# Performance work log

Measured on AMD Instinct MI355X. Metric: run time of the kernel, lower is better.

Reference implementation:

```python
import jax, jax.numpy as jnp
import numpy as np

N_CELLS, N_CLASSES, N_GENES, N_EDGES, HID = 100000, 50, 500, 600000, 8
NEG_SLOPE = 0.2  # GATv2Conv default negative_slope


def setup_inputs() -> dict:
    key = jax.random.key(0)
    ks = jax.random.split(key, 10)
    X = jax.random.normal(ks[0], (N_CELLS, N_GENES), jnp.float32)
    Mu = jax.random.normal(ks[1], (N_CLASSES, N_GENES), jnp.float32)
    # variances must be strictly positive
    Var = jax.random.uniform(ks[2], (N_CLASSES, N_GENES), jnp.float32) + 0.5
    W = 0.1 * jax.random.normal(ks[3], (N_CELLS, N_CLASSES), jnp.float32)
    S = 1.0 + 0.05 * jax.random.normal(ks[4], (N_CELLS, 1), jnp.float32)
    edge_index = jax.random.randint(ks[5], (2, N_EDGES), 0, N_CELLS, jnp.int32)
    sc = 1.0 / np.sqrt(N_GENES)
    lin_l_w = sc * jax.random.normal(ks[6], (HID, N_GENES), jnp.float32)
    lin_l_b = jnp.zeros((HID,), jnp.float32)
    lin_r_w = sc * jax.random.normal(ks[7], (HID, N_GENES), jnp.float32)
    lin_r_b = jnp.zeros((HID,), jnp.float32)
    att = jax.random.normal(ks[8], (HID,), jnp.float32) / np.sqrt(HID)
    return dict(X=X, Mu=Mu, Var=Var, W=W, S=S, edge_index=edge_index,
                lin_l_w=lin_l_w, lin_l_b=lin_l_b,
                lin_r_w=lin_r_w, lin_r_b=lin_r_b, att=att)


def _forward(X, Mu, Var, W, S, lin_l_w, lin_l_b, lin_r_w, lin_r_b, att, edge_index):
    N = X.shape[0]
    P = jax.nn.softmax(W, axis=1)  # [N, C]

    # Gaussian log-likelihood term.
    # F[n,c] = -0.5 * sum_g (X[n,g] - Mu[c,g]*S[n])^2 / Var[c,g]
    # Expanded into GEMMs (algebraically identical, avoids the [N,C,G] intermediate):
    invV = 1.0 / Var                          # [C, G]
    t1 = (X * X) @ invV.T                     # [N, C]  sum_g X^2/Var
    t2 = X @ (Mu * invV).T                    # [N, C]  sum_g X*Mu/Var
    t3 = jnp.sum(Mu * Mu * invV, axis=1)      # [C]     sum_g Mu^2/Var
    Fmat = -0.5 * (t1 - 2.0 * S * t2 + (S * S) * t3[None, :])  # [N, C]
    ll_prot = jnp.sum(P * Fmat) / N

    # GATv2 attention coefficients (heads=1, add_self_loops=False).
    gl = X @ lin_l_w.T + lin_l_b              # [N, HID]  lin_l (source side)
    gr = X @ lin_r_w.T + lin_r_b              # [N, HID]  lin_r (target side)
    src, dst = edge_index[0], edge_index[1]
    e = jax.nn.leaky_relu(gl[src] + gr[dst], NEG_SLOPE)  # [E, HID]
    score = e @ att                                       # [E]
    # segment softmax over destination nodes
    m = jax.ops.segment_max(score, dst, num_segments=N)
    ex = jnp.exp(score - m[dst])
    denom = jax.ops.segment_sum(ex, dst, num_segments=N)
    alpha = ex / denom[dst]                               # [E]

    ce_space = -jnp.sum(P[src] * alpha[:, None] * jnp.log(P[dst] + 1e-8)) / N
    return ll_prot, ce_space, P


def reference(X, Mu, Var, W, S, edge_index, lin_l_w, lin_l_b, lin_r_w, lin_r_b, att):
    return _forward(X, Mu, Var, W, S, lin_l_w, lin_l_b, lin_r_w, lin_r_b, att, edge_index)
```

## Files before the change

### kernel.cpp

```cpp
#include <hip/hip_runtime.h>
#include <math.h>

#define N_CELLS   100000
#define N_CLASSES 50
#define N_GENES   500
#define N_EDGES   600000
#define HID       8
#define NKT       8
#define NB_FUSED  1563
#define NB_CE     391
#define PROWS     56

typedef __attribute__((ext_vector_type(4))) float f32x4;
typedef __attribute__((ext_vector_type(8))) short bf16x8;
typedef __attribute__((ext_vector_type(8))) unsigned short u16x8;

static const size_t OFF_BF    = 0;
static const size_t OFF_T3    = 147456;
static const size_t OFF_GLR   = 147712;
static const size_t OFF_PB    = 6547712;
static const size_t OFF_LQ    = 17747712;
static const size_t OFF_DENOM = 28947712;
static const size_t OFF_NUMER = 29347712;
static const size_t OFF_LLP   = 29747712;
static const size_t OFF_CEP   = 29754112;
static const size_t ZERO_BEG  = OFF_DENOM;
static const size_t ZERO_BYTES= 29747712 - 28947712;

__device__ __forceinline__ ushort f2bf(float f) {
    union { float f; unsigned u; } v; v.f = f;
    unsigned r = v.u + 0x7fffu + ((v.u >> 16) & 1u);
    return (ushort)(r >> 16);
}
__device__ __forceinline__ float bf2f(ushort b) {
    union { unsigned u; float f; } v; v.u = ((unsigned)b) << 16; return v.f;
}
__device__ __forceinline__ unsigned cvt_pk_bf16(float lo, float hi) {
    unsigned r;
    asm("v_cvt_pk_bf16_f32 %0, %1, %2" : "=v"(r) : "v"(lo), "v"(hi));
    return r;
}
__device__ __forceinline__ void gload16(const void* g, void* l) {
    __builtin_amdgcn_global_load_lds(
        (const __attribute__((address_space(1))) unsigned int*)g,
        (__attribute__((address_space(3))) unsigned int*)l,
        16, 0, 0);
}

__global__ __launch_bounds__(256) void k_prep(const float* __restrict__ Var,
                                              const float* __restrict__ Mu,
                                              const float* __restrict__ wl,
                                              const float* __restrict__ wr,
                                              ushort* __restrict__ Bf,
                                              float* __restrict__ t3) {
    if (blockIdx.x < 288) {
        int id = blockIdx.x * 256 + threadIdx.x;
        float v = 0.f;
        if (id < 65536) {
            int e    = id & 7;
            int lane = (id >> 3) & 63;
            int j    = (id >> 9) & 15;
            int kt   = id >> 13;
            int t    = j >> 1, ss = j & 1;
            int s    = kt * 2 + ss;
            int k    = s * 32 + ((lane >> 4) << 3) + e;
            int c    = (t & 3) * 16 + (lane & 15);
            if (k < N_GENES && c < N_CLASSES)
                v = (t < 4) ? 1.0f / Var[c * N_GENES + k]
                            : Mu[c * N_GENES + k] / Var[c * N_GENES + k];
        } else {
            int rem  = id - 65536;
            int e    = rem & 7;
            int lane = (rem >> 3) & 63;
            int s    = rem >> 9;
            int k    = s * 32 + ((lane >> 4) << 3) + e;
            int h    = lane & 15;
            if (k < N_GENES)
                v = (h < HID) ? wl[h * N_GENES + k] : wr[(h - HID) * N_GENES + k];
        }
        Bf[id] = f2bf(v);
    } else {
        int c    = (blockIdx.x - 288) * 4 + (threadIdx.x >> 6);
        int lane = threadIdx.x & 63;
        if (c >= N_CLASSES) return;
        float s = 0.f;
        for (int g = lane; g < N_GENES; g += 64) {
            float m = Mu[c * N_GENES + g];
            s += m * m / Var[c * N_GENES + g];
        }
        #pragma unroll
        for (int off = 32; off; off >>= 1) s += __shfl_xor(s, off);
        if (lane == 0) t3[c] = s;
    }
}

__global__ __launch_bounds__(256) void k_softmax(const float* __restrict__ W,
                                                 float* __restrict__ P,
                                                 ushort* __restrict__ Pb,
                                                 ushort* __restrict__ LQ) {
    int wid  = (blockIdx.x * 256 + threadIdx.x) >> 6;
    int lane = threadIdx.x & 63;
    if (wid >= N_CELLS) return;
    float w = (lane < N_CLASSES) ? W[(size_t)wid * N_CLASSES + lane] : -__builtin_inff();
    float m = w;
    #pragma unroll
    for (int off = 32; off; off >>= 1) m = fmaxf(m, __shfl_xor(m, off));
    float e = (lane < N_CLASSES) ? expf(w - m) : 0.f;
    float s = e;
    #pragma unroll
    for (int off = 32; off; off >>= 1) s += __shfl_xor(s, off);
    float p = e / s;
    if (lane < N_CLASSES) P[(size_t)wid * N_CLASSES + lane] = p;
    if (lane < PROWS) {
        Pb[(size_t)wid * PROWS + lane] = (lane < N_CLASSES) ? f2bf(p) : 0;
        LQ[(size_t)wid * PROWS + lane] = (lane < N_CLASSES) ? f2bf(logf(p + 1e-8f)) : 0;
    }
}

__global__ __launch_bounds__(256, 2) void k_fused(const float* __restrict__ X,
                                                  const float* __restrict__ S,
                                                  const float* __restrict__ P,
                                                  const ushort* __restrict__ Bf,
                                                  const float* __restrict__ t3,
                                                  const float* __restrict__ bl,
                                                  const float* __restrict__ br,
                                                  ushort* __restrict__ glrb,
                                                  float* __restrict__ llp) {
    __shared__ float  ldsA[2][4][16][16][4];
    __shared__ ushort ldsB[2][20][64][8];
    __shared__ float  wsum[4];
    int tid  = threadIdx.x;
    int lane = tid & 63;
    int wv   = tid >> 6;
    int lhi  = lane >> 4;
    int slot = lane & 15;
    int rbase = blockIdx.x * 64 + wv * 16;
    const char* Xc  = (const char*)X;
    const char* Bfc = (const char*)Bf;

    int arow = rbase + slot;
    if (arow > N_CELLS - 1) arow = N_CELLS - 1;
    float m2s = -2.0f * S[arow];

    const f32x4 zz = {0.f, 0.f, 0.f, 0.f};
    f32x4 acc1[4], acc2[4], acc3;
    #pragma unroll
    for (int ct = 0; ct < 4; ++ct) { acc1[ct] = zz; acc2[ct] = zz; }
    acc3 = zz;

#define STAGE(KT, BUF) do {                                                        \
    _Pragma("unroll")                                                              \
    for (int i = 0; i < 4; ++i) {                                                  \
        int rloc = i * 4 + lhi;                                                    \
        int row  = rbase + rloc; if (row > N_CELLS - 1) row = N_CELLS - 1;         \
        int gi   = (KT) * 16 + (slot ^ (rloc & 7)); if (gi > 124) gi = 124;        \
        gload16(Xc + (size_t)row * 2000 + (size_t)gi * 16, &ldsA[BUF][wv][i * 4][0][0]); \
    }                                                                              \
    _Pragma("unroll")                                                              \
    for (int i = 0; i < 5; ++i) {                                                  \
        int j = wv * 5 + i;                                                        \
        size_t src;                                                                \
        if (j < 16)      src = (size_t)(KT) * 16384 + (size_t)j * 1024;            \
        else if (j < 18) src = 131072 + ((size_t)(KT) * 2 + (size_t)(j - 16)) * 1024; \
        else             src = (size_t)(KT) * 16384;                               \
        gload16(Bfc + src + (size_t)lane * 16, &ldsB[BUF][j][0][0]);               \
    }                                                                              \
} while (0)

    STAGE(0, 0);

    #pragma unroll
    for (int kt = 0; kt < NKT; ++kt) {
        const int cur = kt & 1;
        if (kt < NKT - 1) {
            STAGE(kt + 1, cur ^ 1);
            __builtin_amdgcn_sched_barrier(0);
            asm volatile("s_waitcnt vmcnt(9)" ::: "memory");
        } else {
            __builtin_amdgcn_sched_barrier(0);
            asm volatile("s_waitcnt vmcnt(0)" ::: "memory");
        }
        __builtin_amdgcn_sched_barrier(0);
        __builtin_amdgcn_s_barrier();
        __builtin_amdgcn_sched_barrier(0);

        const bf16x8* BL = (const bf16x8*)&ldsB[cur][0][0][0];
        #pragma unroll
        for (int ks = 0; ks < 2; ++ks) {
            int key = slot & 7;
            int c0  = ks * 8 + lhi * 2;
            f32x4 xa = *(const f32x4*)&ldsA[cur][wv][slot][c0 ^ key][0];
            f32x4 xb = *(const f32x4*)&ldsA[cur][wv][slot][(c0 + 1) ^ key][0];
            union { bf16x8 v; unsigned u[4]; } a1, a2;
            a1.u[0] = cvt_pk_bf16(xa[0] * xa[0], xa[1] * xa[1]);
            a1.u[1] = cvt_pk_bf16(xa[2] * xa[2], xa[3] * xa[3]);
            a1.u[2] = cvt_pk_bf16(xb[0] * xb[0], xb[1] * xb[1]);
            a1.u[3] = cvt_pk_bf16(xb[2] * xb[2], xb[3] * xb[3]);
            a2.u[0] = cvt_pk_bf16(m2s * xa[0], m2s * xa[1]);
            a2.u[1] = cvt_pk_bf16(m2s * xa[2], m2s * xa[3]);
            a2.u[2] = cvt_pk_bf16(m2s * xb[0], m2s * xb[1]);
            a2.u[3] = cvt_pk_bf16(m2s * xb[2], m2s * xb[3]);
            bf16x8 bg = BL[(16 + ks) * 64 + lane];
            #pragma unroll
            for (int ct = 0; ct < 4; ++ct)
                acc1[ct] = __builtin_amdgcn_mfma_f32_16x16x32_bf16(a1.v, BL[(ct * 2 + ks) * 64 + lane], acc1[ct], 0, 0, 0);
            #pragma unroll
            for (int ct = 0; ct < 4; ++ct)
                acc2[ct] = __builtin_amdgcn_mfma_f32_16x16x32_bf16(a2.v, BL[((4 + ct) * 2 + ks) * 64 + lane], acc2[ct], 0, 0, 0);
            acc3 = __builtin_amdgcn_mfma_f32_16x16x32_bf16(a2.v, bg, acc3, 0, 0, 0);
        }
        __builtin_amdgcn_sched_barrier(0);
        __builtin_amdgcn_s_barrier();
        __builtin_amdgcn_sched_barrier(0);
    }
#undef STAGE

    int col = lane & 15;
    int rg  = lane >> 4;
    float bias = (col < HID) ? bl[col] : br[col - HID];
    float part = 0.f;
    #pragma unroll
    for (int r = 0; r < 4; ++r) {
        int row = rbase + rg * 4 + r;
        if (row < N_CELLS) {
            float s2 = S[row];
            glrb[(size_t)row * 16 + col] = f2bf(acc3[r] / (-2.0f * s2) + bias);
            float ss = s2 * s2;
            #pragma unroll
            for (int ct = 0; ct < 4; ++ct) {
                int c = ct * 16 + col;
                if (c < N_CLASSES) {
                    float F = -0.5f * (acc1[ct][r] + acc2[ct][r] + ss * t3[c]);
                    part = fmaf(P[(size_t)row * N_CLASSES + c], F, part);
                }
            }
        }
    }
    #pragma unroll
    for (int off = 32; off; off >>= 1) part += __shfl_xor(part, off);
    if (lane == 0) wsum[wv] = part;
    __syncthreads();
    if (tid == 0) llp[blockIdx.x] = wsum[0] + wsum[1] + wsum[2] + wsum[3];
}

__global__ __launch_bounds__(256) void k_edge(const int* __restrict__ ei,
                                              const ushort* __restrict__ glrb,
                                              const float* __restrict__ att,
                                              const ushort* __restrict__ Pb,
                                              const ushort* __restrict__ LQ,
                                              float* __restrict__ denom,
                                              float* __restrict__ numer) {
    int e = blockIdx.x * 256 + threadIdx.x;
    if (e >= N_EDGES) return;
    int src = ei[e], dst = ei[N_EDGES + e];
    u16x8 gv = *(const u16x8*)(glrb + (size_t)src * 16);
    u16x8 hv = *(const u16x8*)(glrb + (size_t)dst * 16 + 8);
    const float4* at = (const float4*)att;
    float4 a0 = at[0], a1 = at[1];
    float t, s = 0.f;
    t = bf2f(gv[0]) + bf2f(hv[0]); t = t > 0.f ? t : 0.2f * t; s = fmaf(a0.x, t, s);
    t = bf2f(gv[1]) + bf2f(hv[1]); t = t > 0.f ? t : 0.2f * t; s = fmaf(a0.y, t, s);
    t = bf2f(gv[2]) + bf2f(hv[2]); t = t > 0.f ? t : 0.2f * t; s = fmaf(a0.z, t, s);
    t = bf2f(gv[3]) + bf2f(hv[3]); t = t > 0.f ? t : 0.2f * t; s = fmaf(a0.w, t, s);
    t = bf2f(gv[4]) + bf2f(hv[4]); t = t > 0.f ? t : 0.2f * t; s = fmaf(a1.x, t, s);
    t = bf2f(gv[5]) + bf2f(hv[5]); t = t > 0.f ? t : 0.2f * t; s = fmaf(a1.y, t, s);
    t = bf2f(gv[6]) + bf2f(hv[6]); t = t > 0.f ? t : 0.2f * t; s = fmaf(a1.z, t, s);
    t = bf2f(gv[7]) + bf2f(hv[7]); t = t > 0.f ? t : 0.2f * t; s = fmaf(a1.w, t, s);
    float ex = expf(s);

    const u16x8* ps = (const u16x8*)(Pb + (size_t)src * PROWS);
    const u16x8* ld = (const u16x8*)(LQ + (size_t)dst * PROWS);
    float v = 0.f;
    #pragma unroll
    for (int i = 0; i < 7; ++i) {
        u16x8 pv = ps[i], lv = ld[i];
        #pragma unroll
        for (int j = 0; j < 8; ++j)
            v = fmaf(bf2f(pv[j]), bf2f(lv[j]), v);
    }
    atomicAdd(denom + dst, ex);
    atomicAdd(numer + dst, ex * v);
}

__global__ __launch_bounds__(256) void k_ce(const float* __restrict__ denom,
                                            const float* __restrict__ numer,
                                            float* __restrict__ cep) {
    __shared__ float wsum[4];
    int n = blockIdx.x * 256 + threadIdx.x;
    float v = 0.f;
    if (n < N_CELLS) {
        float d = denom[n];
        v = (d > 0.f) ? numer[n] / d : 0.f;
    }
    #pragma unroll
    for (int off = 32; off; off >>= 1) v += __shfl_xor(v, off);
    if ((threadIdx.x & 63) == 0) wsum[threadIdx.x >> 6] = v;
    __syncthreads();
    if (threadIdx.x == 0) cep[blockIdx.x] = wsum[0] + wsum[1] + wsum[2] + wsum[3];
}

__global__ __launch_bounds__(256) void k_reduce(const float* __restrict__ llp,
                                                const float* __restrict__ cep,
                                                float* __restrict__ out) {
    __shared__ double l1[256], l2[256];
    int t = threadIdx.x;
    double s1 = 0.0, s2 = 0.0;
    for (int i = t; i < NB_FUSED; i += 256) s1 += (double)llp[i];
    for (int i = t; i < NB_CE; i += 256) s2 += (double)cep[i];
    l1[t] = s1; l2[t] = s2;
    __syncthreads();
    for (int off = 128; off; off >>= 1) {
        if (t < off) { l1[t] += l1[t + off]; l2[t] += l2[t + off]; }
        __syncthreads();
    }
    if (t == 0) {
        out[0] = (float)(l1[0] / (double)N_CELLS);
        out[1] = (float)(-l2[0] / (double)N_CELLS);
    }
}

extern "C" void kernel_launch(void* const* d_in, const int* in_sizes, int n_in,
                              void* d_out, int out_size, void* d_ws, size_t ws_size,
                              hipStream_t stream) {
    const float* X   = (const float*)d_in[0];
    const float* Mu  = (const float*)d_in[1];
    const float* Var = (const float*)d_in[2];
    const float* W   = (const float*)d_in[3];
    const float* S   = (const float*)d_in[4];
    const int*   ei  = (const int*)d_in[5];
    const float* wl  = (const float*)d_in[6];
    const float* bl  = (const float*)d_in[7];
    const float* wr  = (const float*)d_in[8];
    const float* br  = (const float*)d_in[9];
    const float* att = (const float*)d_in[10];
    float* out = (float*)d_out;
    char*  ws  = (char*)d_ws;

    ushort* Bf    = (ushort*)(ws + OFF_BF);
    float*  t3    = (float*)(ws + OFF_T3);
    ushort* glrb  = (ushort*)(ws + OFF_GLR);
    ushort* Pb    = (ushort*)(ws + OFF_PB);
    ushort* LQ    = (ushort*)(ws + OFF_LQ);
    float*  denom = (float*)(ws + OFF_DENOM);
    float*  numer = (float*)(ws + OFF_NUMER);
    float*  llp   = (float*)(ws + OFF_LLP);
    float*  cep   = (float*)(ws + OFF_CEP);
    float*  P     = out + 2;

    hipMemsetAsync(ws + ZERO_BEG, 0, ZERO_BYTES, stream);

    k_prep   <<<301, 256, 0, stream>>>(Var, Mu, wl, wr, Bf, t3);
    k_softmax<<<(N_CELLS * 64 + 255) / 256, 256, 0, stream>>>(W, P, Pb, LQ);
    k_fused  <<<NB_FUSED, 256, 0, stream>>>(X, S, P, Bf, t3, bl, br, glrb, llp);
    k_edge   <<<(N_EDGES + 255) / 256, 256, 0, stream>>>(ei, glrb, att, Pb, LQ, denom, numer);
    k_ce     <<<NB_CE, 256, 0, stream>>>(denom, numer, cep);
    k_reduce <<<1, 256, 0, stream>>>(llp, cep, out);
}
```

Before: 179.1 us.

## Merge prep, softmax and memset into one kernel; fold final reduce via ticket

Replaces the memset, prep and softmax launches with a single k_front kernel. Its first blocks zero the denom/numer accumulators and the ticket, build the bf16 B tiles and t3, and the remaining blocks compute the row softmax. The separate final reduction kernel is removed: the last k_ce block, found with an atomic ticket counter, does the double-precision reduction. This cuts three launches and their inter-kernel gaps, at the cost of threadfence/atomic overhead and a serial tail in the last block.

```diff
diff --git a/kernel.cpp b/kernel.cpp
--- a/kernel.cpp
+++ b/kernel.cpp
@@ -24,8 +24,7 @@
 static const size_t OFF_NUMER = 29347712;
 static const size_t OFF_LLP   = 29747712;
 static const size_t OFF_CEP   = 29754112;
-static const size_t ZERO_BEG  = OFF_DENOM;
-static const size_t ZERO_BYTES= 29747712 - 28947712;
+static const size_t OFF_TKT   = 29755904;
 
 __device__ __forceinline__ ushort f2bf(float f) {
     union { float f; unsigned u; } v; v.f = f;
@@ -47,12 +46,23 @@
         16, 0, 0);
 }
 
-__global__ __launch_bounds__(256) void k_prep(const float* __restrict__ Var,
-                                              const float* __restrict__ Mu,
-                                              const float* __restrict__ wl,
-                                              const float* __restrict__ wr,
-                                              ushort* __restrict__ Bf,
-                                              float* __restrict__ t3) {
+__global__ __launch_bounds__(256) void k_front(const float* __restrict__ Var,
+                                               const float* __restrict__ Mu,
+                                               const float* __restrict__ wl,
+                                               const float* __restrict__ wr,
+                                               const float* __restrict__ W,
+                                               ushort* __restrict__ Bf,
+                                               float* __restrict__ t3,
+                                               float* __restrict__ P,
+                                               ushort* __restrict__ Pb,
+                                               ushort* __restrict__ LQ,
+                                               unsigned* __restrict__ zeroed,
+                                               unsigned* __restrict__ ticket) {
+    if (blockIdx.x < 301) {
+        int gid = blockIdx.x * 256 + threadIdx.x;
+        for (int i = gid; i < 200000; i += 77056) zeroed[i] = 0u;
+        if (gid == 0) *ticket = 0u;
+    }
     if (blockIdx.x < 288) {
         int id = blockIdx.x * 256 + threadIdx.x;
         float v = 0.f;
@@ -79,7 +89,7 @@
                 v = (h < HID) ? wl[h * N_GENES + k] : wr[(h - HID) * N_GENES + k];
         }
         Bf[id] = f2bf(v);
-    } else {
+    } else if (blockIdx.x < 301) {
         int c    = (blockIdx.x - 288) * 4 + (threadIdx.x >> 6);
         int lane = threadIdx.x & 63;
         if (c >= N_CLASSES) return;
@@ -91,29 +101,23 @@
         #pragma unroll
         for (int off = 32; off; off >>= 1) s += __shfl_xor(s, off);
         if (lane == 0) t3[c] = s;
-    }
-}
-
-__global__ __launch_bounds__(256) void k_softmax(const float* __restrict__ W,
-                                                 float* __restrict__ P,
-                                                 ushort* __restrict__ Pb,
-                                                 ushort* __restrict__ LQ) {
-    int wid  = (blockIdx.x * 256 + threadIdx.x) >> 6;
-    int lane = threadIdx.x & 63;
-    if (wid >= N_CELLS) return;
-    float w = (lane < N_CLASSES) ? W[(size_t)wid * N_CLASSES + lane] : -__builtin_inff();
-    float m = w;
-    #pragma unroll
-    for (int off = 32; off; off >>= 1) m = fmaxf(m, __shfl_xor(m, off));
-    float e = (lane < N_CLASSES) ? expf(w - m) : 0.f;
-    float s = e;
-    #pragma unroll
-    for (int off = 32; off; off >>= 1) s += __shfl_xor(s, off);
-    float p = e / s;
-    if (lane < N_CLASSES) P[(size_t)wid * N_CLASSES + lane] = p;
-    if (lane < PROWS) {
-        Pb[(size_t)wid * PROWS + lane] = (lane < N_CLASSES) ? f2bf(p) : 0;
-        LQ[(size_t)wid * PROWS + lane] = (lane < N_CLASSES) ? f2bf(logf(p + 1e-8f)) : 0;
+    } else {
+        int wid  = (blockIdx.x - 301) * 4 + (threadIdx.x >> 6);
+        int lane = threadIdx.x & 63;
+        float w = (lane < N_CLASSES) ? W[(size_t)wid * N_CLASSES + lane] : -__builtin_inff();
+        float m = w;
+        #pragma unroll
+        for (int off = 32; off; off >>= 1) m = fmaxf(m, __shfl_xor(m, off));
+        float e = (lane < N_CLASSES) ? expf(w - m) : 0.f;
+        float s = e;
+        #pragma unroll
+        for (int off = 32; off; off >>= 1) s += __shfl_xor(s, off);
+        float p = e / s;
+        if (lane < N_CLASSES) P[(size_t)wid * N_CLASSES + lane] = p;
+        if (lane < PROWS) {
+            Pb[(size_t)wid * PROWS + lane] = (lane < N_CLASSES) ? f2bf(p) : 0;
+            LQ[(size_t)wid * PROWS + lane] = (lane < N_CLASSES) ? f2bf(logf(p + 1e-8f)) : 0;
+        }
     }
 }
 
@@ -282,10 +286,15 @@
     atomicAdd(numer + dst, ex * v);
 }
 
-__global__ __launch_bounds__(256) void k_ce(const float* __restrict__ denom,
-                                            const float* __restrict__ numer,
-                                            float* __restrict__ cep) {
+__global__ __launch_bounds__(256) void k_ce_final(const float* __restrict__ denom,
+                                                  const float* __restrict__ numer,
+                                                  const float* __restrict__ llp,
+                                                  float* __restrict__ cep,
+                                                  unsigned* __restrict__ ticket,
+                                                  float* __restrict__ out) {
     __shared__ float wsum[4];
+    __shared__ unsigned lastv;
+    __shared__ double l1[256], l2[256];
     int n = blockIdx.x * 256 + threadIdx.x;
     float v = 0.f;
     if (n < N_CELLS) {
@@ -296,26 +305,28 @@
     for (int off = 32; off; off >>= 1) v += __shfl_xor(v, off);
     if ((threadIdx.x & 63) == 0) wsum[threadIdx.x >> 6] = v;
     __syncthreads();
-    if (threadIdx.x == 0) cep[blockIdx.x] = wsum[0] + wsum[1] + wsum[2] + wsum[3];
-}
-
-__global__ __launch_bounds__(256) void k_reduce(const float* __restrict__ llp,
-                                                const float* __restrict__ cep,
-                                                float* __restrict__ out) {
-    __shared__ double l1[256], l2[256];
-    int t = threadIdx.x;
-    double s1 = 0.0, s2 = 0.0;
-    for (int i = t; i < NB_FUSED; i += 256) s1 += (double)llp[i];
-    for (int i = t; i < NB_CE; i += 256) s2 += (double)cep[i];
-    l1[t] = s1; l2[t] = s2;
+    if (threadIdx.x == 0) {
+        cep[blockIdx.x] = wsum[0] + wsum[1] + wsum[2] + wsum[3];
+        __threadfence();
+        lastv = atomicAdd(ticket, 1u);
+    }
     __syncthreads();
-    for (int off = 128; off; off >>= 1) {
-        if (t < off) { l1[t] += l1[t + off]; l2[t] += l2[t + off]; }
+    if (lastv == NB_CE - 1) {
+        __threadfence();
+        int t = threadIdx.x;
+        double s1 = 0.0, s2 = 0.0;
+        for (int i = t; i < NB_FUSED; i += 256) s1 += (double)llp[i];
+        for (int i = t; i < NB_CE; i += 256) s2 += (double)cep[i];
+        l1[t] = s1; l2[t] = s2;
         __syncthreads();
-    }
-    if (t == 0) {
-        out[0] = (float)(l1[0] / (double)N_CELLS);
-        out[1] = (float)(-l2[0] / (double)N_CELLS);
+        for (int off = 128; off; off >>= 1) {
+            if (t < off) { l1[t] += l1[t + off]; l2[t] += l2[t + off]; }
+            __syncthreads();
+        }
+        if (t == 0) {
+            out[0] = (float)(l1[0] / (double)N_CELLS);
+            out[1] = (float)(-l2[0] / (double)N_CELLS);
+        }
     }
 }
 
@@ -336,23 +347,21 @@
     float* out = (float*)d_out;
     char*  ws  = (char*)d_ws;
 
-    ushort* Bf    = (ushort*)(ws + OFF_BF);
-    float*  t3    = (float*)(ws + OFF_T3);
-    ushort* glrb  = (ushort*)(ws + OFF_GLR);
-    ushort* Pb    = (ushort*)(ws + OFF_PB);
-    ushort* LQ    = (ushort*)(ws + OFF_LQ);
-    float*  denom = (float*)(ws + OFF_DENOM);
-    float*  numer = (float*)(ws + OFF_NUMER);
-    float*  llp   = (float*)(ws + OFF_LLP);
-    float*  cep   = (float*)(ws + OFF_CEP);
-    float*  P     = out + 2;
-
-    hipMemsetAsync(ws + ZERO_BEG, 0, ZERO_BYTES, stream);
-
-    k_prep   <<<301, 256, 0, stream>>>(Var, Mu, wl, wr, Bf, t3);
-    k_softmax<<<(N_CELLS * 64 + 255) / 256, 256, 0, stream>>>(W, P, Pb, LQ);
-    k_fused  <<<NB_FUSED, 256, 0, stream>>>(X, S, P, Bf, t3, bl, br, glrb, llp);
-    k_edge   <<<(N_EDGES + 255) / 256, 256, 0, stream>>>(ei, glrb, att, Pb, LQ, denom, numer);
-    k_ce     <<<NB_CE, 256, 0, stream>>>(denom, numer, cep);
-    k_reduce <<<1, 256, 0, stream>>>(llp, cep, out);
-}
+    ushort*   Bf    = (ushort*)(ws + OFF_BF);
+    float*    t3    = (float*)(ws + OFF_T3);
+    ushort*   glrb  = (ushort*)(ws + OFF_GLR);
+    ushort*   Pb    = (ushort*)(ws + OFF_PB);
+    ushort*   LQ    = (ushort*)(ws + OFF_LQ);
+    float*    denom = (float*)(ws + OFF_DENOM);
+    float*    numer = (float*)(ws + OFF_NUMER);
+    float*    llp   = (float*)(ws + OFF_LLP);
+    float*    cep   = (float*)(ws + OFF_CEP);
+    unsigned* tkt   = (unsigned*)(ws + OFF_TKT);
+    float*    P     = out + 2;
+
+    k_front   <<<301 + 25000, 256, 0, stream>>>(Var, Mu, wl, wr, W, Bf, t3, P, Pb, LQ,
+                                                (unsigned*)(ws + OFF_DENOM), tkt);
+    k_fused   <<<NB_FUSED, 256, 0, stream>>>(X, S, P, Bf, t3, bl, br, glrb, llp);
+    k_edge    <<<(N_EDGES + 255) / 256, 256, 0, stream>>>(ei, glrb, att, Pb, LQ, denom, numer);
+    k_ce_final<<<NB_CE, 256, 0, stream>>>(denom, numer, llp, cep, tkt, out);
+}
```

Result: no change. 175.9 us (median of 2 runs) (-1.8%).
